# Performance work log

Hardware: AMD Instinct MI355X
Metric: run time of the kernel (lower is better)

The kernel has to match this reference:

```python
import jax, jax.numpy as jnp
import numpy as np
from jax.ops import segment_sum, segment_max

N, F, H, HEADS, E, OUT = 50000, 256, 64, 4, 800000, 16


def setup_inputs() -> dict:
    key = jax.random.key(0)
    ks = jax.random.split(key, 16)
    s = 0.05
    return {
        "x": jax.random.normal(ks[0], (N, F), jnp.float32),
        "edge_index": jax.random.randint(ks[1], (2, E), 0, N, jnp.int64),
        # GCN layer params
        "W_gcn1": jax.random.normal(ks[2], (F, H), jnp.float32) * s,
        "b_gcn1": jnp.zeros((H,), jnp.float32),
        "W_gcn2": jax.random.normal(ks[3], (H, OUT), jnp.float32) * s,
        "b_gcn2": jnp.zeros((OUT,), jnp.float32),
        # GAT layer 1 (heads=HEADS, concat)
        "W_gat1": jax.random.normal(ks[4], (F, HEADS * H), jnp.float32) * s,
        "a_src1": jax.random.normal(ks[5], (HEADS, H), jnp.float32) * s,
        "a_dst1": jax.random.normal(ks[6], (HEADS, H), jnp.float32) * s,
        "b_gat1": jnp.zeros((HEADS * H,), jnp.float32),
        # GAT layer 2 (heads=1, concat=False)
        "W_gat2": jax.random.normal(ks[7], (HEADS * H, OUT), jnp.float32) * s,
        "a_src2": jax.random.normal(ks[8], (1, OUT), jnp.float32) * s,
        "a_dst2": jax.random.normal(ks[9], (1, OUT), jnp.float32) * s,
        "b_gat2": jnp.zeros((OUT,), jnp.float32),
    }


def _add_self_loops(edge_index, n):
    loop = jnp.arange(n, dtype=edge_index.dtype)
    src = jnp.concatenate([edge_index[0], loop])
    dst = jnp.concatenate([edge_index[1], loop])
    return src, dst


def _gcn(x, src, dst, norm, W, b, n):
    h = x @ W  # [N, out]
    out = segment_sum(h[src] * norm[:, None], dst, num_segments=n)
    return out + b


def _gat(x, src, dst, W, a_s, a_d, b, heads, concat, n):
    h = (x @ W).reshape(n, heads, -1)  # [N, heads, C]
    s_src = jnp.einsum("nhc,hc->nh", h, a_s)
    s_dst = jnp.einsum("nhc,hc->nh", h, a_d)
    e = jax.nn.leaky_relu(s_src[src] + s_dst[dst], 0.2)  # [Etot, heads]
    m = segment_max(e, dst, num_segments=n)               # per-dst softmax
    p = jnp.exp(e - m[dst])
    denom = segment_sum(p, dst, num_segments=n)
    alpha = p / denom[dst]
    out = segment_sum(h[src] * alpha[..., None], dst, num_segments=n)
    out = out.reshape(n, -1) if concat else out.mean(axis=1)
    return out + b


def reference(x, edge_index, W_gcn1, b_gcn1, W_gcn2, b_gcn2,
              W_gat1, a_src1, a_dst1, b_gat1,
              W_gat2, a_src2, a_dst2, b_gat2):
    n = x.shape[0]
    src, dst = _add_self_loops(edge_index, n)
    # symmetric GCN normalization on self-loop-augmented graph
    deg = segment_sum(jnp.ones_like(dst, x.dtype), dst, num_segments=n)
    dinv = jnp.where(deg > 0, jax.lax.rsqrt(deg), 0.0)
    norm = dinv[src] * dinv[dst]

    x_gcn = jax.nn.relu(_gcn(x, src, dst, norm, W_gcn1, b_gcn1, n))
    x_gcn = _gcn(x_gcn, src, dst, norm, W_gcn2, b_gcn2, n)

    x_gat = jax.nn.relu(_gat(x, src, dst, W_gat1, a_src1, a_dst1, b_gat1, HEADS, True, n))
    x_gat = _gat(x_gat, src, dst, W_gat2, a_src2, a_dst2, b_gat2, 1, False, n)

    return jnp.concatenate([x_gcn, x_gat], axis=1)
```

## Files before the change

kernel.cpp:

```cpp
#include <hip/hip_runtime.h>
#include <math.h>

#define NN     50000
#define FF     256
#define HH     64
#define NHEADS 4
#define EE     800000
#define OUTD   16

typedef __attribute__((ext_vector_type(8))) short short8;
typedef __attribute__((ext_vector_type(4))) float f32x4;

__device__ inline unsigned short f2bf(float f) {
    unsigned u = __builtin_bit_cast(unsigned, f);
    unsigned r = (u + 0x7fff + ((u >> 16) & 1)) >> 16;
    return (unsigned short)r;
}
__device__ inline float bf2f(unsigned short s) {
    unsigned u = ((unsigned)s) << 16;
    return __builtin_bit_cast(float, u);
}

__device__ inline void pack_one(const float* __restrict__ W,
                                unsigned short* __restrict__ bhi,
                                unsigned short* __restrict__ blo,
                                int t_, int NT, int NTOT, int TOFF, int SRC_NC) {
    int lane = t_ & 63;
    int tile = (t_ >> 6) % NT;
    int kb = (t_ >> 6) / NT;
    int q = lane >> 4, c = lane & 15;
    size_t off = ((size_t)(kb * NTOT + TOFF + tile) * 64 + lane) * 8;
#pragma unroll
    for (int j = 0; j < 8; j++) {
        float w = W[(size_t)(kb * 32 + q * 8 + j) * SRC_NC + tile * 16 + c];
        unsigned short h = f2bf(w);
        bhi[off + j] = h;
        if (blo) blo[off + j] = f2bf(w - bf2f(h));
    }
}

#define NTT 20
__global__ __launch_bounds__(256) void k_prep(const float* __restrict__ Wg1,
                                              const float* __restrict__ Wgat1,
                                              const float* __restrict__ Wg2,
                                              const float* __restrict__ Wgat2,
                                              unsigned short* __restrict__ bhiC,
                                              unsigned short* __restrict__ bhiG2,
                                              unsigned short* __restrict__ bloG2,
                                              unsigned short* __restrict__ bhiA2,
                                              unsigned short* __restrict__ bloA2,
                                              int* __restrict__ cnt) {
    int t = blockIdx.x * 256 + threadIdx.x;
    if (t < NN) cnt[t] = 0;
    if (t < 2048)        pack_one(Wg1,   bhiC,  nullptr, t,         4,  NTT, 0, 64);
    else if (t < 10240)  pack_one(Wgat1, bhiC,  nullptr, t - 2048,  16, NTT, 4, 256);
    else if (t < 10368)  pack_one(Wg2,   bhiG2, bloG2,   t - 10240, 1,  1,   0, 16);
    else if (t < 10880)  pack_one(Wgat2, bhiA2, bloA2,   t - 10368, 1,  1,   0, 16);
}

__global__ void k_count(const int* __restrict__ dst, int* __restrict__ cnt, int e) {
    int i = blockIdx.x * blockDim.x + threadIdx.x;
    if (i < e) atomicAdd(&cnt[dst[i]], 1);
}

__global__ __launch_bounds__(256) void k_scan_a(const int* __restrict__ cnt,
                                                int* __restrict__ partial, int n) {
    int i = blockIdx.x * 256 + threadIdx.x;
    int v = (i < n) ? cnt[i] : 0;
#pragma unroll
    for (int off = 32; off >= 1; off >>= 1) v += __shfl_xor(v, off, 64);
    __shared__ int ws[4];
    int wave = threadIdx.x >> 6;
    if ((threadIdx.x & 63) == 0) ws[wave] = v;
    __syncthreads();
    if (threadIdx.x == 0) partial[blockIdx.x] = ws[0] + ws[1] + ws[2] + ws[3];
}

__global__ __launch_bounds__(256) void k_scan_b(const int* __restrict__ partial,
                                                int* __restrict__ blockoff,
                                                int* __restrict__ total_out, int nb) {
    __shared__ int arr[256];
    int tid = threadIdx.x;
    arr[tid] = (tid < nb) ? partial[tid] : 0;
    __syncthreads();
#pragma unroll
    for (int off = 1; off < 256; off <<= 1) {
        int v = arr[tid];
        int add = (tid >= off) ? arr[tid - off] : 0;
        __syncthreads();
        arr[tid] = v + add;
        __syncthreads();
    }
    if (tid < nb) blockoff[tid] = arr[tid] - partial[tid];
    if (tid == 0) *total_out = arr[255];
}

__global__ __launch_bounds__(256) void k_scan_c(const int* __restrict__ cnt,
                                                const int* __restrict__ blockoff,
                                                int* __restrict__ row_start,
                                                int* __restrict__ cursor,
                                                float* __restrict__ dinv, int n) {
    __shared__ int arr[256];
    int tid = threadIdx.x;
    int i = blockIdx.x * 256 + tid;
    int c = (i < n) ? cnt[i] : 0;
    arr[tid] = c;
    __syncthreads();
#pragma unroll
    for (int off = 1; off < 256; off <<= 1) {
        int v = arr[tid];
        int add = (tid >= off) ? arr[tid - off] : 0;
        __syncthreads();
        arr[tid] = v + add;
        __syncthreads();
    }
    if (i < n) {
        int excl = arr[tid] - c + blockoff[blockIdx.x];
        row_start[i] = excl;
        cursor[i] = excl;
        dinv[i] = rsqrtf((float)(c + 1));
    }
}

__global__ void k_fill(const int* __restrict__ src, const int* __restrict__ dst,
                       int* __restrict__ cursor, int* __restrict__ col, int e) {
    int i = blockIdx.x * blockDim.x + threadIdx.x;
    if (i < e) {
        int d = dst[i];
        int pos = atomicAdd(&cursor[d], 1);
        col[pos] = src[i];
    }
}

__global__ __launch_bounds__(256, 4) void mfma_gemm_fused(const float* __restrict__ A,
                                                       const unsigned short* __restrict__ Bhi,
                                                       unsigned short* __restrict__ Ch1,
                                                       unsigned char* __restrict__ Chg,
                                                       float* __restrict__ scl,
                                                       const float* __restrict__ dinv,
                                                       const float* __restrict__ a_s,
                                                       const float* __restrict__ a_d,
                                                       float* __restrict__ ssrc,
                                                       float* __restrict__ sdst,
                                                       int M) {
    const int K = 256;
    int tid = threadIdx.x;
    int w = tid >> 6, lane = tid & 63, q = lane >> 4, c = lane & 15;
    int row_base = blockIdx.x * 64 + w * 16;
    int ar = min(row_base + c, M - 1);
    const float* ap = A + (size_t)ar * K + q * 8;
    const short8* bp = (const short8*)Bhi + lane;

    f32x4 acc[NTT];
#pragma unroll
    for (int t = 0; t < NTT; t++) acc[t] = (f32x4){0.f, 0.f, 0.f, 0.f};

    float av[8];
    *(float4*)(av)     = *(const float4*)(ap);
    *(float4*)(av + 4) = *(const float4*)(ap + 4);
#pragma unroll
    for (int kb = 0; kb < 8; kb++) {
        short8 ahi, alo;
#pragma unroll
        for (int j = 0; j < 8; j++) {
            unsigned short h = f2bf(av[j]);
            ahi[j] = (short)h;
            alo[j] = (short)f2bf(av[j] - bf2f(h));
        }
        if (kb < 7) {
            *(float4*)(av)     = *(const float4*)(ap + (kb + 1) * 32);
            *(float4*)(av + 4) = *(const float4*)(ap + (kb + 1) * 32 + 4);
        }
#pragma unroll
        for (int t = 0; t < NTT; t++) {
            short8 bhi = bp[(size_t)(kb * NTT + t) * 64];
            acc[t] = __builtin_amdgcn_mfma_f32_16x16x32_bf16(ahi, bhi, acc[t], 0, 0, 0);
            acc[t] = __builtin_amdgcn_mfma_f32_16x16x32_bf16(alo, bhi, acc[t], 0, 0, 0);
        }
    }

#pragma unroll
    for (int i = 0; i < 4; i++) {
        int r = row_base + q * 4 + i;
        float ss[4] = {0.f, 0.f, 0.f, 0.f};
        float sd[4] = {0.f, 0.f, 0.f, 0.f};
#pragma unroll
        for (int t = 0; t < 16; t++) {
            float v = acc[t + 4][i];
            ss[t >> 2] += v * a_s[t * 16 + c];
            sd[t >> 2] += v * a_d[t * 16 + c];
        }
#pragma unroll
        for (int h = 0; h < 4; h++) {
#pragma unroll
            for (int off = 1; off <= 8; off <<= 1) {
                ss[h] += __shfl_xor(ss[h], off, 16);
                sd[h] += __shfl_xor(sd[h], off, 16);
            }
        }
        if (c == i && r < M) {
            *(float4*)(ssrc + (size_t)r * 4) = make_float4(ss[0], ss[1], ss[2], ss[3]);
            *(float4*)(sdst + (size_t)r * 4) = make_float4(sd[0], sd[1], sd[2], sd[3]);
        }
    }

#pragma unroll
    for (int i = 0; i < 4; i++) {
        int r = row_base + q * 4 + i;
        float m = 0.f;
#pragma unroll
        for (int t = 0; t < 16; t++) m = fmaxf(m, fabsf(acc[t + 4][i]));
#pragma unroll
        for (int off = 1; off <= 8; off <<= 1) m = fmaxf(m, __shfl_xor(m, off, 16));
        m = fmaxf(m, 1e-20f);
        float inv = 127.0f / m;
        if (c == i && r < M) scl[r] = m * (1.0f / 127.0f);
        if (r < M) {
            float sc = dinv[r];
#pragma unroll
            for (int t = 0; t < 4; t++)
                Ch1[(size_t)r * 64 + t * 16 + c] = f2bf(acc[t][i] * sc);
#pragma unroll
            for (int t = 0; t < 16; t++) {
                int qv = (int)rintf(acc[t + 4][i] * inv) + 128;
                Chg[(size_t)r * 256 + t * 16 + c] = (unsigned char)qv;
            }
        }
    }
}

template <int KB, bool SCALE, bool SC2, int OFS>
__device__ inline void n16_body(int bx, int tid,
                                const unsigned short* __restrict__ A,
                                const unsigned short* __restrict__ Bhi,
                                const unsigned short* __restrict__ Blo,
                                unsigned short* __restrict__ Cbf,
                                const float* __restrict__ rowscale,
                                const float* __restrict__ a_s2,
                                const float* __restrict__ a_d2,
                                float* __restrict__ s2s,
                                float* __restrict__ s2d, int M) {
    const int K = KB * 32;
    int w = tid >> 6, lane = tid & 63, q = lane >> 4, c = lane & 15;
    int row_base = bx * 64 + w * 16;
    int ar = min(row_base + c, M - 1);
    const unsigned short* ap = A + (size_t)ar * K + q * 8;
    f32x4 acc = (f32x4){0.f, 0.f, 0.f, 0.f};
#pragma unroll
    for (int kb = 0; kb < KB; kb++) {
        short8 av = *(const short8*)(ap + kb * 32);
        size_t bo = ((size_t)kb * 64 + lane) * 8;
        short8 bh = *(const short8*)(Bhi + bo);
        short8 bl = *(const short8*)(Blo + bo);
        acc = __builtin_amdgcn_mfma_f32_16x16x32_bf16(av, bh, acc, 0, 0, 0);
        acc = __builtin_amdgcn_mfma_f32_16x16x32_bf16(av, bl, acc, 0, 0, 0);
    }
    if (SC2) {
#pragma unroll
        for (int i = 0; i < 4; i++) {
            float ps = acc[i] * a_s2[c];
            float pd = acc[i] * a_d2[c];
#pragma unroll
            for (int off = 1; off <= 8; off <<= 1) {
                ps += __shfl_xor(ps, off, 16);
                pd += __shfl_xor(pd, off, 16);
            }
            int r = row_base + q * 4 + i;
            if (c == i && r < M) {
                s2s[r] = ps;
                s2d[r] = pd;
            }
        }
    }
#pragma unroll
    for (int i = 0; i < 4; i++) {
        int r = row_base + q * 4 + i;
        if (r < M) {
            float sc = SCALE ? rowscale[r] : 1.0f;
            Cbf[((size_t)r * 16 + c) * 2 + OFS] = f2bf(acc[i] * sc);
        }
    }
}

__global__ __launch_bounds__(256) void mfma_n16_both(const unsigned short* __restrict__ Ag,
                                                     const unsigned short* __restrict__ Ac,
                                                     const unsigned short* __restrict__ bhiA2,
                                                     const unsigned short* __restrict__ bloA2,
                                                     const unsigned short* __restrict__ bhiG2,
                                                     const unsigned short* __restrict__ bloG2,
                                                     unsigned short* __restrict__ pairb,
                                                     const float* __restrict__ dinv,
                                                     const float* __restrict__ a_s2,
                                                     const float* __restrict__ a_d2,
                                                     float* __restrict__ s2s,
                                                     float* __restrict__ s2d,
                                                     int M, int GB) {
    int bx = blockIdx.x;
    if (bx < GB)
        n16_body<8, false, true, 1>(bx, threadIdx.x, Ag, bhiA2, bloA2, pairb,
                                    nullptr, a_s2, a_d2, s2s, s2d, M);
    else
        n16_body<2, true, false, 0>(bx - GB, threadIdx.x, Ac, bhiG2, bloG2, pairb,
                                    dinv, nullptr, nullptr, nullptr, nullptr, M);
}

__global__ __launch_bounds__(256) void both_agg(const unsigned char* __restrict__ hg,
                                                const unsigned short* __restrict__ h1,
                                                const float* __restrict__ scl,
                                                const int* __restrict__ rs,
                                                const int* __restrict__ col,
                                                const float* __restrict__ ssrc,
                                                const float* __restrict__ sdst,
                                                const float* __restrict__ dinv,
                                                const float* __restrict__ bgat,
                                                const float* __restrict__ bgcn,
                                                unsigned short* __restrict__ outg,
                                                unsigned short* __restrict__ outc) {
    __shared__ int s_lds[4][64];
    __shared__ float p_lds[4][64 * 4];
    int tid = threadIdx.x;
    int w = tid >> 6, lane = tid & 63;
    int wid = blockIdx.x * 4 + w;
    int hh = lane >> 4;
    int cidx = (lane & 15) * 4;
    int* sl = s_lds[w];
    float* pl = p_lds[w];

    float di = dinv[wid];
    float4 sd4 = *(const float4*)(sdst + (size_t)wid * 4);
    float sdv[4] = {sd4.x, sd4.y, sd4.z, sd4.w};
    float4 sf4 = *(const float4*)(ssrc + (size_t)wid * 4);
    float sfv[4] = {sf4.x, sf4.y, sf4.z, sf4.w};
    float psf[4];
#pragma unroll
    for (int h = 0; h < 4; h++) {
        float e = sfv[h] + sdv[h];
        e = (e >= 0.f) ? e : 0.2f * e;
        psf[h] = __expf(e);
    }
    float pse = (hh & 2) ? ((hh & 1) ? psf[3] : psf[2]) : ((hh & 1) ? psf[1] : psf[0]);
    float pses = pse * scl[wid];
    const unsigned char* hbase = hg + lane * 4;
    unsigned hv0 = *(const unsigned*)(hbase + (size_t)wid * 256);
    float4 acc;
    acc.x = ((float)(hv0 & 0xffu) - 128.f) * pses;
    acc.y = ((float)((hv0 >> 8) & 0xffu) - 128.f) * pses;
    acc.z = ((float)((hv0 >> 16) & 0xffu) - 128.f) * pses;
    acc.w = ((float)(hv0 >> 24) - 128.f) * pses;
    float accb = 0.f;
    float4 accc = make_float4(0.f, 0.f, 0.f, 0.f);

    float lsum[4] = {0.f, 0.f, 0.f, 0.f};
    int beg = rs[wid], end = rs[wid + 1];
    for (int j0 = beg; j0 < end; j0 += 64) {
        int cnt = min(64, end - j0);
        if (lane < cnt) {
            int sreg = col[j0 + lane];
            float ssc = scl[sreg];
            float4 sv = *(const float4*)(ssrc + (size_t)sreg * 4);
            float svv[4] = {sv.x, sv.y, sv.z, sv.w};
            float pv[4];
#pragma unroll
            for (int h = 0; h < 4; h++) {
                float e = svv[h] + sdv[h];
                e = (e >= 0.f) ? e : 0.2f * e;
                pv[h] = __expf(e);
                lsum[h] += pv[h];
            }
            sl[lane] = sreg;
            *(float4*)&pl[lane * 4] =
                make_float4(pv[0] * ssc, pv[1] * ssc, pv[2] * ssc, pv[3] * ssc);
        }
        int e = 0;
        for (; e + 4 <= cnt; e += 4) {
            int s0 = sl[e], s1 = sl[e + 1], s2 = sl[e + 2], s3 = sl[e + 3];
            float p0 = pl[e * 4 + hh], p1 = pl[(e + 1) * 4 + hh];
            float p2 = pl[(e + 2) * 4 + hh], p3 = pl[(e + 3) * 4 + hh];
            unsigned v0 = *(const unsigned*)(hbase + (size_t)s0 * 256);
            unsigned v1 = *(const unsigned*)(hbase + (size_t)s1 * 256);
            unsigned v2 = *(const unsigned*)(hbase + (size_t)s2 * 256);
            unsigned v3 = *(const unsigned*)(hbase + (size_t)s3 * 256);
            acc.x += (float)(v0 & 0xffu) * p0;
            acc.y += (float)((v0 >> 8) & 0xffu) * p0;
            acc.z += (float)((v0 >> 16) & 0xffu) * p0;
            acc.w += (float)(v0 >> 24) * p0;
            acc.x += (float)(v1 & 0xffu) * p1;
            acc.y += (float)((v1 >> 8) & 0xffu) * p1;
            acc.z += (float)((v1 >> 16) & 0xffu) * p1;
            acc.w += (float)(v1 >> 24) * p1;
            acc.x += (float)(v2 & 0xffu) * p2;
            acc.y += (float)((v2 >> 8) & 0xffu) * p2;
            acc.z += (float)((v2 >> 16) & 0xffu) * p2;
            acc.w += (float)(v2 >> 24) * p2;
            acc.x += (float)(v3 & 0xffu) * p3;
            acc.y += (float)((v3 >> 8) & 0xffu) * p3;
            acc.z += (float)((v3 >> 16) & 0xffu) * p3;
            acc.w += (float)(v3 >> 24) * p3;
            accb += (p0 + p1) + (p2 + p3);
        }
        for (; e < cnt; e++) {
            int s = sl[e];
            float p = pl[e * 4 + hh];
            unsigned v = *(const unsigned*)(hbase + (size_t)s * 256);
            acc.x += (float)(v & 0xffu) * p;
            acc.y += (float)((v >> 8) & 0xffu) * p;
            acc.z += (float)((v >> 16) & 0xffu) * p;
            acc.w += (float)(v >> 24) * p;
            accb += p;
        }
        int e2 = hh;
        for (; e2 + 4 < cnt; e2 += 8) {
            int sa = sl[e2], sb = sl[e2 + 4];
            ushort4 va = *(const ushort4*)(h1 + (size_t)sa * HH + cidx);
            ushort4 vb = *(const ushort4*)(h1 + (size_t)sb * HH + cidx);
            accc.x += bf2f(va.x) + bf2f(vb.x);
            accc.y += bf2f(va.y) + bf2f(vb.y);
            accc.z += bf2f(va.z) + bf2f(vb.z);
            accc.w += bf2f(va.w) + bf2f(vb.w);
        }
        if (e2 < cnt) {
            int sa = sl[e2];
            ushort4 va = *(const ushort4*)(h1 + (size_t)sa * HH + cidx);
            accc.x += bf2f(va.x); accc.y += bf2f(va.y);
            accc.z += bf2f(va.z); accc.w += bf2f(va.w);
        }
    }
    float corr = 128.0f * accb;
    acc.x -= corr; acc.y -= corr; acc.z -= corr; acc.w -= corr;
#pragma unroll
    for (int h = 0; h < 4; h++) {
        float v = lsum[h];
        for (int off = 32; off >= 1; off >>= 1) v += __shfl_xor(v, off, 64);
        lsum[h] = v + psf[h];
    }
    float lt = (hh & 2) ? ((hh & 1) ? lsum[3] : lsum[2]) : ((hh & 1) ? lsum[1] : lsum[0]);
    float li = 1.0f / lt;
    float4 bv = *(const float4*)(bgat + lane * 4);
    ushort4 o;
    o.x = f2bf(fmaxf(acc.x * li + bv.x, 0.f));
    o.y = f2bf(fmaxf(acc.y * li + bv.y, 0.f));
    o.z = f2bf(fmaxf(acc.z * li + bv.z, 0.f));
    o.w = f2bf(fmaxf(acc.w * li + bv.w, 0.f));
    *(ushort4*)(outg + (size_t)wid * 256 + lane * 4) = o;
#pragma unroll
    for (int off = 16; off <= 32; off <<= 1) {
        accc.x += __shfl_xor(accc.x, off, 64);
        accc.y += __shfl_xor(accc.y, off, 64);
        accc.z += __shfl_xor(accc.z, off, 64);
        accc.w += __shfl_xor(accc.w, off, 64);
    }
    if (hh == 0) {
        ushort4 sv = *(const ushort4*)(h1 + (size_t)wid * HH + cidx);
        float4 bc = *(const float4*)(bgcn + cidx);
        ushort4 oc;
        oc.x = f2bf(fmaxf((accc.x + bf2f(sv.x)) * di + bc.x, 0.f));
        oc.y = f2bf(fmaxf((accc.y + bf2f(sv.y)) * di + bc.y, 0.f));
        oc.z = f2bf(fmaxf((accc.z + bf2f(sv.z)) * di + bc.z, 0.f));
        oc.w = f2bf(fmaxf((accc.w + bf2f(sv.w)) * di + bc.w, 0.f));
        *(ushort4*)(outc + (size_t)wid * HH + cidx) = oc;
    }
}

__global__ __launch_bounds__(256) void final_agg(const unsigned* __restrict__ hp,
                                                 const int* __restrict__ rs,
                                                 const int* __restrict__ col,
                                                 const float* __restrict__ dinv,
                                                 const float* __restrict__ s2s,
                                                 const float* __restrict__ s2d,
                                                 const float* __restrict__ bg2,
                                                 const float* __restrict__ bga2,
                                                 float* __restrict__ out) {
    int t = blockIdx.x * 256 + threadIdx.x;
    int node = t >> 4;
    int c = t & 15;
    float di = dinv[node];
    float sd = s2d[node];
    float es = s2s[node] + sd;
    es = (es >= 0.f) ? es : 0.2f * es;
    float psf = __expf(es);
    unsigned pvs = hp[(size_t)node * 16 + c];
    float accg = bf2f((unsigned short)pvs);
    float acca = bf2f((unsigned short)(pvs >> 16)) * psf;
    float lp = 0.f;
    int beg = rs[node], end = rs[node + 1];
    for (int j0 = beg; j0 < end; j0 += 16) {
        int cnt = min(16, end - j0);
        int sreg = 0;
        float pr = 0.f;
        if (c < cnt) {
            sreg = col[j0 + c];
            float e = s2s[sreg] + sd;
            e = (e >= 0.f) ? e : 0.2f * e;
            pr = __expf(e);
            lp += pr;
        }
        for (int e = 0; e < cnt; e += 4) {
            int si[4];
            float pi[4];
#pragma unroll
            for (int u = 0; u < 4; u++) {
                si[u] = __shfl(sreg, (e + u) & 15, 16);
                pi[u] = __shfl(pr, (e + u) & 15, 16);
            }
            unsigned hv[4];
#pragma unroll
            for (int u = 0; u < 4; u++) hv[u] = hp[(size_t)si[u] * 16 + c];
#pragma unroll
            for (int u = 0; u < 4; u++) {
                if (e + u < cnt) {
                    accg += bf2f((unsigned short)hv[u]);
                    acca += bf2f((unsigned short)(hv[u] >> 16)) * pi[u];
                }
            }
        }
    }
    for (int off = 8; off >= 1; off >>= 1) lp += __shfl_xor(lp, off, 16);
    float l = lp + psf;
    out[(size_t)node * 32 + c] = accg * di + bg2[c];
    out[(size_t)node * 32 + 16 + c] = acca / l + bga2[c];
}

extern "C" void kernel_launch(void* const* d_in, const int* in_sizes, int n_in,
                              void* d_out, int out_size, void* d_ws, size_t ws_size,
                              hipStream_t stream) {
    const float* x      = (const float*)d_in[0];
    const int*   ei     = (const int*)d_in[1];
    const float* Wg1    = (const float*)d_in[2];
    const float* bg1    = (const float*)d_in[3];
    const float* Wg2    = (const float*)d_in[4];
    const float* bg2    = (const float*)d_in[5];
    const float* Wgat1  = (const float*)d_in[6];
    const float* a_src1 = (const float*)d_in[7];
    const float* a_dst1 = (const float*)d_in[8];
    const float* bgat1  = (const float*)d_in[9];
    const float* Wgat2  = (const float*)d_in[10];
    const float* a_src2 = (const float*)d_in[11];
    const float* a_dst2 = (const float*)d_in[12];
    const float* bgat2  = (const float*)d_in[13];
    float* out = (float*)d_out;

    const int* e_src = ei;
    const int* e_dst = ei + EE;

    char* wsb = (char*)d_ws;
    size_t o = 0;
    auto alloc = [&](size_t bytes) -> void* {
        void* p = wsb + o;
        o += (bytes + 255) & ~(size_t)255;
        return p;
    };
    float* dinv            = (float*)alloc(NN * 4);
    float* ssrc1           = (float*)alloc((size_t)NN * 16);
    float* sdst1           = (float*)alloc((size_t)NN * 16);
    unsigned short* h1b    = (unsigned short*)alloc((size_t)NN * HH * 2);
    unsigned short* xg1    = (unsigned short*)alloc((size_t)NN * HH * 2);
    unsigned char*  hgb    = (unsigned char*)alloc((size_t)NN * 256);
    float* sclb            = (float*)alloc(NN * 4);
    unsigned short* xgat1  = (unsigned short*)alloc((size_t)NN * 256 * 2);
    unsigned short* pairb  = (unsigned short*)alloc((size_t)NN * 16 * 4);
    float* s2src           = (float*)alloc(NN * 4);
    float* s2dst           = (float*)alloc(NN * 4);
    unsigned short* bhiC   = (unsigned short*)alloc((size_t)8 * NTT * 512 * 2);
    unsigned short* bhiG2  = (unsigned short*)alloc(64 * 16 * 2);
    unsigned short* bloG2  = (unsigned short*)alloc(64 * 16 * 2);
    unsigned short* bhiA2  = (unsigned short*)alloc(256 * 16 * 2);
    unsigned short* bloA2  = (unsigned short*)alloc(256 * 16 * 2);
    int* cnt               = (int*)alloc(NN * 4);
    int* rowstart          = (int*)alloc((NN + 1) * 4);
    int* cursor            = (int*)alloc(NN * 4);
    int* colarr            = (int*)alloc((size_t)EE * 4);
    int* partial           = (int*)alloc(256 * 4);
    int* blockoff          = (int*)alloc(256 * 4);

    const int TB = 256;
    const int NB = (NN + 255) / 256;
    k_prep<<<NB, TB, 0, stream>>>(Wg1, Wgat1, Wg2, Wgat2,
                                  bhiC, bhiG2, bloG2, bhiA2, bloA2, cnt);
    k_count<<<(EE + TB - 1) / TB, TB, 0, stream>>>(e_dst, cnt, EE);
    k_scan_a<<<NB, TB, 0, stream>>>(cnt, partial, NN);
    k_scan_b<<<1, TB, 0, stream>>>(partial, blockoff, rowstart + NN, NB);
    k_scan_c<<<NB, TB, 0, stream>>>(cnt, blockoff, rowstart, cursor, dinv, NN);
    k_fill<<<(EE + TB - 1) / TB, TB, 0, stream>>>(e_src, e_dst, cursor, colarr, EE);

    const int GB = (NN + 63) / 64;
    const int G16 = (NN * 16) / 256;

    mfma_gemm_fused<<<GB, TB, 0, stream>>>(x, bhiC, h1b, hgb, sclb, dinv,
                                           a_src1, a_dst1, ssrc1, sdst1, NN);

    both_agg<<<NN / 4, TB, 0, stream>>>(hgb, h1b, sclb, rowstart, colarr, ssrc1, sdst1,
                                        dinv, bgat1, bg1, xgat1, xg1);

    mfma_n16_both<<<2 * GB, TB, 0, stream>>>(xgat1, xg1, bhiA2, bloA2, bhiG2, bloG2,
                                             pairb, dinv, a_src2, a_dst2,
                                             s2src, s2dst, NN, GB);

    final_agg<<<G16, TB, 0, stream>>>((const unsigned*)pairb, rowstart, colarr, dinv,
                                      s2src, s2dst, bg2, bgat2, out);
}
```

Measured before the change: 350.1 us.

## Split fused GEMM output columns across two wave halves per block

The first-layer fused GEMM now launches 512 threads per block, and each half of the waves computes 10 of the 20 output column tiles for the same 64 rows. This halves the accumulator registers per wave and doubles the number of waves available to hide latency. Per-row attention scores and abs-max partials are combined through shared memory after a block barrier. The cost is that each A row is loaded and converted to bf16 twice, plus a __syncthreads.

```diff
diff --git a/kernel.cpp b/kernel.cpp
--- a/kernel.cpp
+++ b/kernel.cpp
@@ -132,7 +132,7 @@
     }
 }
 
-__global__ __launch_bounds__(256, 4) void mfma_gemm_fused(const float* __restrict__ A,
+__global__ __launch_bounds__(512, 4) void mfma_gemm_fused(const float* __restrict__ A,
                                                        const unsigned short* __restrict__ Bhi,
                                                        unsigned short* __restrict__ Ch1,
                                                        unsigned char* __restrict__ Chg,
@@ -146,14 +146,17 @@
     const int K = 256;
     int tid = threadIdx.x;
     int w = tid >> 6, lane = tid & 63, q = lane >> 4, c = lane & 15;
-    int row_base = blockIdx.x * 64 + w * 16;
+    int rg = w & 3;
+    int half = w >> 2;
+    const int T0 = half * 10;
+    int row_base = blockIdx.x * 64 + rg * 16;
     int ar = min(row_base + c, M - 1);
     const float* ap = A + (size_t)ar * K + q * 8;
     const short8* bp = (const short8*)Bhi + lane;
 
-    f32x4 acc[NTT];
-#pragma unroll
-    for (int t = 0; t < NTT; t++) acc[t] = (f32x4){0.f, 0.f, 0.f, 0.f};
+    f32x4 acc[10];
+#pragma unroll
+    for (int t = 0; t < 10; t++) acc[t] = (f32x4){0.f, 0.f, 0.f, 0.f};
 
     float av[8];
     *(float4*)(av)     = *(const float4*)(ap);
@@ -172,23 +175,33 @@
             *(float4*)(av + 4) = *(const float4*)(ap + (kb + 1) * 32 + 4);
         }
 #pragma unroll
-        for (int t = 0; t < NTT; t++) {
-            short8 bhi = bp[(size_t)(kb * NTT + t) * 64];
-            acc[t] = __builtin_amdgcn_mfma_f32_16x16x32_bf16(ahi, bhi, acc[t], 0, 0, 0);
-            acc[t] = __builtin_amdgcn_mfma_f32_16x16x32_bf16(alo, bhi, acc[t], 0, 0, 0);
-        }
-    }
+        for (int lt = 0; lt < 10; lt++) {
+            short8 bhi = bp[(size_t)(kb * NTT + T0 + lt) * 64];
+            acc[lt] = __builtin_amdgcn_mfma_f32_16x16x32_bf16(ahi, bhi, acc[lt], 0, 0, 0);
+            acc[lt] = __builtin_amdgcn_mfma_f32_16x16x32_bf16(alo, bhi, acc[lt], 0, 0, 0);
+        }
+    }
+
+    __shared__ float s_ss[2][64][4];
+    __shared__ float s_sd[2][64][4];
+    __shared__ float s_mx[2][64];
 
 #pragma unroll
     for (int i = 0; i < 4; i++) {
-        int r = row_base + q * 4 + i;
+        int lr = rg * 16 + q * 4 + i;
         float ss[4] = {0.f, 0.f, 0.f, 0.f};
         float sd[4] = {0.f, 0.f, 0.f, 0.f};
-#pragma unroll
-        for (int t = 0; t < 16; t++) {
-            float v = acc[t + 4][i];
-            ss[t >> 2] += v * a_s[t * 16 + c];
-            sd[t >> 2] += v * a_d[t * 16 + c];
+        float m = 0.f;
+#pragma unroll
+        for (int lt = 0; lt < 10; lt++) {
+            int gt = T0 + lt;
+            if (gt >= 4) {
+                int t = gt - 4;
+                float v = acc[lt][i];
+                ss[t >> 2] += v * a_s[t * 16 + c];
+                sd[t >> 2] += v * a_d[t * 16 + c];
+                m = fmaxf(m, fabsf(v));
+            }
         }
 #pragma unroll
         for (int h = 0; h < 4; h++) {
@@ -198,32 +211,49 @@
                 sd[h] += __shfl_xor(sd[h], off, 16);
             }
         }
-        if (c == i && r < M) {
-            *(float4*)(ssrc + (size_t)r * 4) = make_float4(ss[0], ss[1], ss[2], ss[3]);
-            *(float4*)(sdst + (size_t)r * 4) = make_float4(sd[0], sd[1], sd[2], sd[3]);
-        }
-    }
+#pragma unroll
+        for (int off = 1; off <= 8; off <<= 1) m = fmaxf(m, __shfl_xor(m, off, 16));
+        if (c == i) {
+#pragma unroll
+            for (int h = 0; h < 4; h++) {
+                s_ss[half][lr][h] = ss[h];
+                s_sd[half][lr][h] = sd[h];
+            }
+            s_mx[half][lr] = m;
+        }
+    }
+    __syncthreads();
 
 #pragma unroll
     for (int i = 0; i < 4; i++) {
+        int lr = rg * 16 + q * 4 + i;
         int r = row_base + q * 4 + i;
-        float m = 0.f;
-#pragma unroll
-        for (int t = 0; t < 16; t++) m = fmaxf(m, fabsf(acc[t + 4][i]));
-#pragma unroll
-        for (int off = 1; off <= 8; off <<= 1) m = fmaxf(m, __shfl_xor(m, off, 16));
-        m = fmaxf(m, 1e-20f);
+        float m = fmaxf(fmaxf(s_mx[0][lr], s_mx[1][lr]), 1e-20f);
         float inv = 127.0f / m;
-        if (c == i && r < M) scl[r] = m * (1.0f / 127.0f);
+        if (half == 0 && c == i && r < M) {
+            *(float4*)(ssrc + (size_t)r * 4) =
+                make_float4(s_ss[0][lr][0] + s_ss[1][lr][0], s_ss[0][lr][1] + s_ss[1][lr][1],
+                            s_ss[0][lr][2] + s_ss[1][lr][2], s_ss[0][lr][3] + s_ss[1][lr][3]);
+            *(float4*)(sdst + (size_t)r * 4) =
+                make_float4(s_sd[0][lr][0] + s_sd[1][lr][0], s_sd[0][lr][1] + s_sd[1][lr][1],
+                            s_sd[0][lr][2] + s_sd[1][lr][2], s_sd[0][lr][3] + s_sd[1][lr][3]);
+            scl[r] = m * (1.0f / 127.0f);
+        }
         if (r < M) {
-            float sc = dinv[r];
-#pragma unroll
-            for (int t = 0; t < 4; t++)
-                Ch1[(size_t)r * 64 + t * 16 + c] = f2bf(acc[t][i] * sc);
-#pragma unroll
-            for (int t = 0; t < 16; t++) {
-                int qv = (int)rintf(acc[t + 4][i] * inv) + 128;
-                Chg[(size_t)r * 256 + t * 16 + c] = (unsigned char)qv;
+            if (half == 0) {
+                float sc = dinv[r];
+#pragma unroll
+                for (int lt = 0; lt < 4; lt++)
+                    Ch1[(size_t)r * 64 + lt * 16 + c] = f2bf(acc[lt][i] * sc);
+            }
+#pragma unroll
+            for (int lt = 0; lt < 10; lt++) {
+                int gt = T0 + lt;
+                if (gt >= 4) {
+                    int t = gt - 4;
+                    int qv = (int)rintf(acc[lt][i] * inv) + 128;
+                    Chg[(size_t)r * 256 + t * 16 + c] = (unsigned char)qv;
+                }
             }
         }
     }
@@ -585,8 +615,8 @@
     const int GB = (NN + 63) / 64;
     const int G16 = (NN * 16) / 256;
 
-    mfma_gemm_fused<<<GB, TB, 0, stream>>>(x, bhiC, h1b, hgb, sclb, dinv,
-                                           a_src1, a_dst1, ssrc1, sdst1, NN);
+    mfma_gemm_fused<<<GB, 512, 0, stream>>>(x, bhiC, h1b, hgb, sclb, dinv,
+                                            a_src1, a_dst1, ssrc1, sdst1, NN);
 
     both_agg<<<NN / 4, TB, 0, stream>>>(hgb, h1b, sclb, rowstart, colarr, ssrc1, sdst1,
                                         dinv, bgat1, bg1, xgat1, xg1);
```

After: 340.5 us. 1.03x faster.
